# Performance work log

Hardware: AMD Instinct MI355X
Metric: run time of the kernel (lower is better)

Reference implementation:

```python
import jax, jax.numpy as jnp
import numpy as np

NEG_INF = -1e30  # masked_softmax fill (squad util convention)


def setup_inputs() -> dict:
    key = jax.random.key(0)
    ks = jax.random.split(key, 5)
    B, S, H = 4, 2048, 512
    x = jax.random.normal(ks[0], (B, S, H), dtype=jnp.float32)
    mask = jax.random.randint(ks[1], (B, S), 0, 2, dtype=jnp.int32)
    mask = mask.at[:, 0].set(1)  # ensure at least one valid key per row
    W_comb = jax.random.normal(ks[2], (H, 3 * H), dtype=jnp.float32) * (1.0 / np.sqrt(H))
    b_comb = jnp.zeros((3 * H,), dtype=jnp.float32)
    W_out = jax.random.normal(ks[3], (H, H), dtype=jnp.float32) * (1.0 / np.sqrt(H))
    b_out = jnp.zeros((H,), dtype=jnp.float32)
    return {"x": x, "mask": mask, "W_comb": W_comb, "b_comb": b_comb,
            "W_out": W_out, "b_out": b_out}


def reference(x, mask, W_comb, b_comb, W_out, b_out):
    B, S, H = x.shape
    n_head = 8
    d = H // n_head
    scale = d ** 0.5
    qkv = x @ W_comb + b_comb                      # [B,S,3H]
    q, k, v = jnp.split(qkv, 3, axis=-1)
    q = q.reshape(B, S, n_head, d)
    k = k.reshape(B, S, n_head, d)
    v = v.reshape(B, S, n_head, d)
    # [B,h,Sq,Sk] scores; mask applies along the key axis
    scores = jnp.einsum('bqhd,bkhd->bhqk', q / scale, k)
    key_mask = (mask > 0)[:, None, None, :]        # [B,1,1,Sk]
    logits = jnp.where(key_mask, scores, NEG_INF)
    attn = jax.nn.softmax(logits, axis=-1)         # dropout = identity (eval)
    out = jnp.einsum('bhqk,bkhd->bqhd', attn, v).reshape(B, S, H)
    return out @ W_out + b_out
```

## Files before the change

### kernel.cpp

```cpp
#include <hip/hip_runtime.h>
#include <hip/hip_bf16.h>
#include <stdint.h>

typedef unsigned short u16;
typedef unsigned int u32;
typedef __attribute__((ext_vector_type(8))) __bf16 bf16x8;
typedef __attribute__((ext_vector_type(8))) unsigned short us8;
typedef __attribute__((ext_vector_type(4))) unsigned short us4;
typedef __attribute__((ext_vector_type(4))) float f32x4;
typedef __attribute__((ext_vector_type(16))) float f32x16;
typedef __attribute__((ext_vector_type(4))) unsigned int u32x4;
typedef __attribute__((ext_vector_type(2))) unsigned int u32x2;

#define KSCALE_Q 0.18033688011112042f

#define VMCNT(n) asm volatile("s_waitcnt vmcnt(" #n ")" ::: "memory")
#define BARRIER() __builtin_amdgcn_s_barrier()

__device__ inline u16 f2bf(float f) {
  union { __bf16 b; u16 s; } x; x.b = (__bf16)f; return x.s;
}
__device__ inline u32 packbf(float a, float b) {
  return (u32)f2bf(a) | ((u32)f2bf(b) << 16);
}
__device__ inline f32x16 zero16() {
  f32x16 z; for (int i = 0; i < 16; ++i) z[i] = 0.f; return z;
}
__device__ __forceinline__ void gl_lds16(const u16* g, u16* l) {
  __builtin_amdgcn_global_load_lds(
      (const __attribute__((address_space(1))) void*)g,
      (__attribute__((address_space(3))) void*)l, 16, 0, 0);
}
__device__ __forceinline__ void pl32swap(u32& a, u32& b) {
#if __has_builtin(__builtin_amdgcn_permlane32_swap)
  u32x2 r = __builtin_amdgcn_permlane32_swap(a, b, false, false);
  a = r[0]; b = r[1];
#else
  u32 ta = (u32)__shfl_xor((int)a, 32);
  u32 tb = (u32)__shfl_xor((int)b, 32);
  int hi = (threadIdx.x & 63) >> 5;
  u32 na = hi ? tb : a;
  u32 nb = hi ? b : ta;
  a = na; b = nb;
#endif
}

__global__ __launch_bounds__(256) void prep(
    const float* __restrict__ x, const float* __restrict__ Wc,
    const float* __restrict__ Wo, const int* __restrict__ mask,
    u16* __restrict__ xbf, u16* __restrict__ wct, u16* __restrict__ wot,
    int* __restrict__ idx, int* __restrict__ nbv) {
  int r = blockIdx.x, tid = threadIdx.x;
  if (r < 4096) {
    int i = r * 256 + tid;
    float4 v = ((const float4*)x)[i];
    us4 o;
    o[0] = f2bf(v.x); o[1] = f2bf(v.y); o[2] = f2bf(v.z); o[3] = f2bf(v.w);
    ((us4*)xbf)[i] = o;
    return;
  }
  __shared__ float tile[32][33];
  __shared__ int ps[256];
  if (r < 5120) {
    const float* in; u16* outT; int R, C, bi;
    if (r < 4864) { in = Wc; outT = wct; R = 512; C = 1536; bi = r - 4096; }
    else          { in = Wo; outT = wot; R = 512; C = 512;  bi = r - 4864; }
    int nbx = C >> 5;
    int bx = bi % nbx, by = bi / nbx;
    int xq = tid & 31, yq = tid >> 5;
    int c0 = bx * 32, r0 = by * 32;
    for (int j = 0; j < 32; j += 8)
      tile[yq + j][xq] = in[(size_t)(r0 + yq + j) * C + c0 + xq];
    __syncthreads();
    for (int j = 0; j < 32; j += 8)
      outT[(size_t)(c0 + yq + j) * R + r0 + xq] = f2bf(tile[xq][yq + j]);
    return;
  }
  int b = r - 5120;
  const int* mrow = mask + b * 2048;
  int4 a = ((const int4*)mrow)[tid * 2];
  int4 c = ((const int4*)mrow)[tid * 2 + 1];
  int v[8] = {a.x, a.y, a.z, a.w, c.x, c.y, c.z, c.w};
  int cnt = 0;
  for (int i = 0; i < 8; ++i) cnt += (v[i] > 0);
  ps[tid] = cnt;
  __syncthreads();
  for (int off = 1; off < 256; off <<= 1) {
    int xv = ps[tid];
    int yv = (tid >= off) ? ps[tid - off] : 0;
    __syncthreads();
    ps[tid] = xv + yv;
    __syncthreads();
  }
  int total = ps[255];
  int pos = ps[tid] - cnt;
  int* ip = idx + b * 2048;
  for (int i = 0; i < 8; ++i)
    if (v[i] > 0) ip[pos++] = tid * 8 + i;
  for (int i = 0; i < 8; ++i) {
    int j = tid * 8 + i;
    if (j >= total) ip[j] = 0;
  }
  if (tid == 0) nbv[b] = total;
}

__global__ __launch_bounds__(256) void gemm_qkv(
    const u16* __restrict__ A, const u16* __restrict__ Bt,
    const float* __restrict__ bias, u16* __restrict__ Qc,
    u16* __restrict__ Kc, u16* __restrict__ VTc,
    const int* __restrict__ idx, const int* __restrict__ nbv) {
  const int K = 512;
  int bid = blockIdx.x;
  bool isQ = bid < 256;
  int b = 0, m0, n0;
  if (isQ) {
    m0 = (bid >> 2) * 128;
    n0 = (bid & 3) * 128;
  } else {
    int t = bid - 256;
    b = t >> 7;
    int rr_ = t & 127;
    m0 = (rr_ & 15) * 128;
    n0 = (rr_ >> 4) * 128 + 512;
    int npad = (nbv[b] + 127) & ~127;
    if (m0 >= npad) return;
  }
  __shared__ __align__(16) u16 As[2][128 * 64];
  __shared__ __align__(16) u16 Bs[2][128 * 64];
  int tid = threadIdx.x, wave = tid >> 6, lane = tid & 63;
  int quad = lane >> 4, l16 = lane & 15;
  int wm = (wave >> 1) * 64, wn = (wave & 1) * 64;

  int r8 = lane >> 3;
  int cb = (lane & 7) ^ r8;
  const u16* agp[4];
  for (int i = 0; i < 4; ++i) {
    int row = m0 + wave * 32 + i * 8 + r8;
    int grow = isQ ? row : (b * 2048 + idx[b * 2048 + row]);
    agp[i] = A + (size_t)grow * K + cb * 8;
  }
  const u16* bg = Bt + (size_t)(n0 + wave * 32 + r8) * K + cb * 8;
  int lofs = (wave * 32) * 64 + lane * 8;

  f32x4 acc[4][4];
  for (int i = 0; i < 4; ++i)
    for (int j = 0; j < 4; ++j) acc[i][j] = (f32x4){0.f, 0.f, 0.f, 0.f};

  int rx = l16 & 7;

  auto stage = [&](int buf, int kk) {
    u16* al = As[buf] + lofs;
    u16* bl = Bs[buf] + lofs;
#pragma unroll
    for (int i = 0; i < 4; ++i)
      gl_lds16(agp[i] + kk, al + i * 8 * 64);
#pragma unroll
    for (int i = 0; i < 4; ++i)
      gl_lds16(bg + kk + (size_t)(i * 8) * K, bl + i * 8 * 64);
  };

  stage(0, 0);
  for (int t = 0; t < 8; ++t) {
    if (t < 7) { stage((t + 1) & 1, (t + 1) * 64); VMCNT(8); }
    else       { VMCNT(0); }
    BARRIER();
    const u16* Asb = As[t & 1];
    const u16* Bsb = Bs[t & 1];
#pragma unroll
    for (int ks = 0; ks < 2; ++ks) {
      int pos = ((ks * 4 + quad) ^ rx) * 8;
      bf16x8 af[4], bfr[4];
#pragma unroll
      for (int i = 0; i < 4; ++i)
        af[i] = *(const bf16x8*)(Asb + (wm + i * 16 + l16) * 64 + pos);
#pragma unroll
      for (int j = 0; j < 4; ++j)
        bfr[j] = *(const bf16x8*)(Bsb + (wn + j * 16 + l16) * 64 + pos);
#pragma unroll
      for (int i = 0; i < 4; ++i)
#pragma unroll
        for (int j = 0; j < 4; ++j)
          acc[i][j] = __builtin_amdgcn_mfma_f32_16x16x32_bf16(
              af[i], bfr[j], acc[i][j], 0, 0, 0);
    }
    BARRIER();
  }
  for (int j = 0; j < 4; ++j) {
    int col = n0 + wn + j * 16 + l16;
    float bv = bias[col];
    if (isQ) {
      for (int i = 0; i < 4; ++i) {
        int rowb = m0 + wm + i * 16 + quad * 4;
        for (int rr = 0; rr < 4; ++rr)
          Qc[(size_t)(rowb + rr) * 512 + col] =
              f2bf((acc[i][j][rr] + bv) * KSCALE_Q);
      }
    } else if (col < 1024) {
      int ck = col - 512;
      for (int i = 0; i < 4; ++i) {
        int key0 = m0 + wm + i * 16 + quad * 4;
        for (int rr = 0; rr < 4; ++rr)
          Kc[((size_t)b * 2048 + key0 + rr) * 512 + ck] =
              f2bf(acc[i][j][rr] + bv);
      }
    } else {
      int hd = col - 1024;
      int h = hd >> 6, d = hd & 63;
      u16* vrow = VTc + ((size_t)(b * 8 + h) * 64 + d) * 2048;
      for (int i = 0; i < 4; ++i) {
        int key0 = m0 + wm + i * 16 + quad * 4;
        us4 pk;
        for (int rr = 0; rr < 4; ++rr) pk[rr] = f2bf(acc[i][j][rr] + bv);
        *(us4*)(vrow + key0) = pk;
      }
    }
  }
}

__global__ __launch_bounds__(256) void gemm_out(
    const u16* __restrict__ A, const u16* __restrict__ Bt,
    const float* __restrict__ bias, float* __restrict__ Cout) {
  const int K = 512, N = 512;
  int m0 = blockIdx.y * 128, n0 = blockIdx.x * 128;
  __shared__ __align__(16) u16 As[2][128 * 64];
  __shared__ __align__(16) u16 Bs[2][128 * 64];
  int tid = threadIdx.x, wave = tid >> 6, lane = tid & 63;
  int quad = lane >> 4, l16 = lane & 15;
  int wm = (wave >> 1) * 64, wn = (wave & 1) * 64;

  int r8 = lane >> 3;
  int cb = (lane & 7) ^ r8;
  const u16* ag = A + (size_t)(m0 + wave * 32 + r8) * K + cb * 8;
  const u16* bg = Bt + (size_t)(n0 + wave * 32 + r8) * K + cb * 8;
  int lofs = (wave * 32) * 64 + lane * 8;

  f32x4 acc[4][4];
  for (int i = 0; i < 4; ++i)
    for (int j = 0; j < 4; ++j) acc[i][j] = (f32x4){0.f, 0.f, 0.f, 0.f};

  int rx = l16 & 7;

  auto stage = [&](int buf, int kk) {
    u16* al = As[buf] + lofs;
    u16* bl = Bs[buf] + lofs;
#pragma unroll
    for (int i = 0; i < 4; ++i)
      gl_lds16(ag + kk + (size_t)(i * 8) * K, al + i * 8 * 64);
#pragma unroll
    for (int i = 0; i < 4; ++i)
      gl_lds16(bg + kk + (size_t)(i * 8) * K, bl + i * 8 * 64);
  };

  stage(0, 0);
  for (int t = 0; t < 8; ++t) {
    if (t < 7) { stage((t + 1) & 1, (t + 1) * 64); VMCNT(8); }
    else       { VMCNT(0); }
    BARRIER();
    const u16* Asb = As[t & 1];
    const u16* Bsb = Bs[t & 1];
#pragma unroll
    for (int ks = 0; ks < 2; ++ks) {
      int pos = ((ks * 4 + quad) ^ rx) * 8;
      bf16x8 af[4], bfr[4];
#pragma unroll
      for (int i = 0; i < 4; ++i)
        af[i] = *(const bf16x8*)(Asb + (wm + i * 16 + l16) * 64 + pos);
#pragma unroll
      for (int j = 0; j < 4; ++j)
        bfr[j] = *(const bf16x8*)(Bsb + (wn + j * 16 + l16) * 64 + pos);
#pragma unroll
      for (int i = 0; i < 4; ++i)
#pragma unroll
        for (int j = 0; j < 4; ++j)
          acc[i][j] = __builtin_amdgcn_mfma_f32_16x16x32_bf16(
              af[i], bfr[j], acc[i][j], 0, 0, 0);
    }
    BARRIER();
  }
  for (int j = 0; j < 4; ++j) {
    int col = n0 + wn + j * 16 + l16;
    float bv = bias[col];
    for (int i = 0; i < 4; ++i) {
      int rowb = m0 + wm + i * 16 + quad * 4;
      for (int rr = 0; rr < 4; ++rr)
        Cout[(size_t)(rowb + rr) * N + col] = acc[i][j][rr] + bv;
    }
  }
}

__global__ __launch_bounds__(256) void attn_kernel(
    const u16* __restrict__ Qc, const u16* __restrict__ Kc,
    const u16* __restrict__ VTc, const int* __restrict__ nbv,
    u16* __restrict__ aout) {
  int b = blockIdx.z, h = blockIdx.y, q0 = blockIdx.x * 256;
  int bh = b * 8 + h;
  int tid = threadIdx.x, wave = tid >> 6, lane = tid & 63;
  int l5 = lane & 31, hi = lane >> 5;
  int nb = nbv[b];
  int npad = (nb + 127) & ~127;
  int NT = npad >> 7;

  __shared__ __align__(16) u16 Kt[2][128 * 64];
  __shared__ __align__(16) u16 Vt[2][64 * 128];

  bf16x8 qf[2][4];
#pragma unroll
  for (int qg = 0; qg < 2; ++qg) {
    int qrow = b * 2048 + q0 + wave * 64 + qg * 32 + l5;
#pragma unroll
    for (int s = 0; s < 4; ++s)
      qf[qg][s] = *(const bf16x8*)(Qc + (size_t)qrow * 512 + h * 64 + s * 16 +
                                   hi * 8);
  }
  VMCNT(0);

  f32x16 o[2][2];
#pragma unroll
  for (int qg = 0; qg < 2; ++qg)
#pragma unroll
    for (int dc = 0; dc < 2; ++dc) o[qg][dc] = zero16();
  float lsum[2] = {0.f, 0.f};

  int krr = lane >> 3;
  int kcb = (lane & 7) ^ krr;
  const u16* kg = Kc + ((size_t)(b * 2048) + wave * 32 + krr) * 512 + h * 64 +
                  kcb * 8;
  int vrr = lane >> 4;

  auto stageKV = [&](int buf, int kt0) {
    u16* kl = Kt[buf] + (wave * 32) * 64 + lane * 8;
#pragma unroll
    for (int i = 0; i < 4; ++i)
      gl_lds16(kg + (size_t)(kt0 + i * 8) * 512, kl + i * 8 * 64);
    u16* vl = Vt[buf] + (wave * 16) * 128 + lane * 8;
#pragma unroll
    for (int i = 0; i < 4; ++i) {
      int vr = wave * 16 + i * 4 + vrr;
      int vcb = (lane & 15) ^ (vr & 15);
      gl_lds16(VTc + ((size_t)(bh * 64) + vr) * 2048 + kt0 + vcb * 8,
               vl + i * 4 * 128);
    }
  };

  stageKV(0, 0);
  for (int t = 0; t < NT; ++t) {
    if (t + 1 < NT) { stageKV((t + 1) & 1, (t + 1) * 128); VMCNT(8); }
    else            { VMCNT(0); }
    BARRIER();
    const u16* Ktc = Kt[t & 1];
    const u16* Vtc = Vt[t & 1];
    int kt0 = t * 128;
    bool maskT = (kt0 + 128 > nb);

#pragma unroll
    for (int kg4 = 0; kg4 < 4; ++kg4) {
      int krow = kg4 * 32 + l5;
      const u16* kro = Ktc + krow * 64;
      int rx = krow & 7;
      bf16x8 ka[4];
#pragma unroll
      for (int s = 0; s < 4; ++s)
        ka[s] = *(const bf16x8*)(kro + ((s * 2 + hi) ^ rx) * 8);
      f32x16 sa[2];
      sa[0] = zero16(); sa[1] = zero16();
#pragma unroll
      for (int s = 0; s < 4; ++s) {
        sa[0] = __builtin_amdgcn_mfma_f32_32x32x16_bf16(ka[s], qf[0][s],
                                                        sa[0], 0, 0, 0);
        sa[1] = __builtin_amdgcn_mfma_f32_32x32x16_bf16(ka[s], qf[1][s],
                                                        sa[1], 0, 0, 0);
      }
      bf16x8 pb[2][2];
#pragma unroll
      for (int qg = 0; qg < 2; ++qg) {
        if (maskT) {
#pragma unroll
          for (int r = 0; r < 16; ++r) {
            int jg = kt0 + kg4 * 32 + (r & 3) + 8 * (r >> 2) + 4 * hi;
            if (jg >= nb) sa[qg][r] = -1e30f;
          }
        }
        u32 pk[8];
        float ls = 0.f;
#pragma unroll
        for (int j = 0; j < 8; ++j) {
          float e0 = __builtin_amdgcn_exp2f(sa[qg][2 * j]);
          float e1 = __builtin_amdgcn_exp2f(sa[qg][2 * j + 1]);
          ls += e0 + e1;
          pk[j] = packbf(e0, e1);
        }
        lsum[qg] += ls;
#pragma unroll
        for (int t2 = 0; t2 < 2; ++t2) {
          u32 a0 = pk[t2 * 4 + 0], a2 = pk[t2 * 4 + 2];
          u32 a1 = pk[t2 * 4 + 1], a3 = pk[t2 * 4 + 3];
          pl32swap(a0, a2);
          pl32swap(a1, a3);
          u32x4 qv; qv[0] = a0; qv[1] = a1; qv[2] = a2; qv[3] = a3;
          pb[qg][t2] = __builtin_bit_cast(bf16x8, qv);
        }
      }
#pragma unroll
      for (int t2 = 0; t2 < 2; ++t2) {
        int cblk = kg4 * 4 + t2 * 2 + hi;
#pragma unroll
        for (int dc = 0; dc < 2; ++dc) {
          int vrow = dc * 32 + l5;
          bf16x8 va = *(const bf16x8*)(Vtc + vrow * 128 +
                                       ((cblk ^ (vrow & 15)) * 8));
          o[0][dc] = __builtin_amdgcn_mfma_f32_32x32x16_bf16(
              va, pb[0][t2], o[0][dc], 0, 0, 0);
          o[1][dc] = __builtin_amdgcn_mfma_f32_32x32x16_bf16(
              va, pb[1][t2], o[1][dc], 0, 0, 0);
        }
      }
    }
    BARRIER();
  }

#pragma unroll
  for (int qg = 0; qg < 2; ++qg) {
    float lt = lsum[qg];
    lt += __shfl_xor(lt, 32);
    float inv = 1.f / lt;
    int qrow = b * 2048 + q0 + wave * 64 + qg * 32 + l5;
#pragma unroll
    for (int dc = 0; dc < 2; ++dc)
#pragma unroll
      for (int mI = 0; mI < 4; ++mI) {
        us4 pk;
        for (int r = 0; r < 4; ++r) pk[r] = f2bf(o[qg][dc][mI * 4 + r] * inv);
        *(us4*)(aout + (size_t)qrow * 512 + h * 64 + dc * 32 + mI * 8 +
                hi * 4) = pk;
      }
  }
}

extern "C" void kernel_launch(void* const* d_in, const int* in_sizes, int n_in,
                              void* d_out, int out_size, void* d_ws,
                              size_t ws_size, hipStream_t stream) {
  const float* x = (const float*)d_in[0];
  const int* mask = (const int*)d_in[1];
  const float* Wc = (const float*)d_in[2];
  const float* bc = (const float*)d_in[3];
  const float* Wo = (const float*)d_in[4];
  const float* bo = (const float*)d_in[5];
  float* out = (float*)d_out;

  char* ws = (char*)d_ws;
  u16* xbf = (u16*)(ws);
  u16* wct = (u16*)(ws + 8388608);
  u16* wot = (u16*)(ws + 9961472);
  u16* Qc  = (u16*)(ws + 10485760);
  u16* Kc  = (u16*)(ws + 18874368);
  u16* vtc = (u16*)(ws + 27262976);
  int* idx = (int*)(ws + 35651584);
  int* nbv = (int*)(ws + 35684352);
  u16* aout = xbf;

  prep<<<5124, 256, 0, stream>>>(x, Wc, Wo, mask, xbf, wct, wot, idx, nbv);
  gemm_qkv<<<768, 256, 0, stream>>>(xbf, wct, bc, Qc, Kc, vtc, idx, nbv);
  attn_kernel<<<dim3(8, 8, 4), 256, 0, stream>>>(Qc, Kc, vtc, nbv, aout);
  gemm_out<<<dim3(4, 64), 256, 0, stream>>>(aout, wot, bo, out);
}
```

Measured before the change: 152.4 us.

## Split attention key range across two wave groups with LDS reduction

Doubles the attention block to 512 threads. The two groups of four waves each process half of the key tiles for the same 256 queries, with separate double-buffered K/V tiles in shared memory. Partial outputs and row sums from the second group are then reduced through shared memory before normalisation and the store. This targets low occupancy: only 256 blocks of 4 waves were available on a large GPU. The cost is doubled LDS per block, an extra reduction pass, and barriers that are now shared across both groups.

```diff
diff --git a/kernel.cpp b/kernel.cpp
--- a/kernel.cpp
+++ b/kernel.cpp
@@ -288,25 +288,29 @@
   }
 }
 
-__global__ __launch_bounds__(256) void attn_kernel(
+__global__ __launch_bounds__(512, 2) void attn_kernel(
     const u16* __restrict__ Qc, const u16* __restrict__ Kc,
     const u16* __restrict__ VTc, const int* __restrict__ nbv,
     u16* __restrict__ aout) {
   int b = blockIdx.z, h = blockIdx.y, q0 = blockIdx.x * 256;
   int bh = b * 8 + h;
   int tid = threadIdx.x, wave = tid >> 6, lane = tid & 63;
+  int g = wave >> 2, sw = wave & 3;
   int l5 = lane & 31, hi = lane >> 5;
   int nb = nbv[b];
   int npad = (nb + 127) & ~127;
   int NT = npad >> 7;
-
-  __shared__ __align__(16) u16 Kt[2][128 * 64];
-  __shared__ __align__(16) u16 Vt[2][64 * 128];
+  int NT0 = (NT + 1) >> 1;
+  int NTg = g ? (NT - NT0) : NT0;
+  int tb = g ? NT0 : 0;
+
+  __shared__ __align__(16) u16 Kt[2][2][128 * 64];
+  __shared__ __align__(16) u16 Vt[2][2][64 * 128];
 
   bf16x8 qf[2][4];
 #pragma unroll
   for (int qg = 0; qg < 2; ++qg) {
-    int qrow = b * 2048 + q0 + wave * 64 + qg * 32 + l5;
+    int qrow = b * 2048 + q0 + sw * 64 + qg * 32 + l5;
 #pragma unroll
     for (int s = 0; s < 4; ++s)
       qf[qg][s] = *(const bf16x8*)(Qc + (size_t)qrow * 512 + h * 64 + s * 16 +
@@ -323,116 +327,154 @@
 
   int krr = lane >> 3;
   int kcb = (lane & 7) ^ krr;
-  const u16* kg = Kc + ((size_t)(b * 2048) + wave * 32 + krr) * 512 + h * 64 +
+  const u16* kg = Kc + ((size_t)(b * 2048) + sw * 32 + krr) * 512 + h * 64 +
                   kcb * 8;
   int vrr = lane >> 4;
 
   auto stageKV = [&](int buf, int kt0) {
-    u16* kl = Kt[buf] + (wave * 32) * 64 + lane * 8;
+    u16* kl = Kt[g][buf] + (sw * 32) * 64 + lane * 8;
 #pragma unroll
     for (int i = 0; i < 4; ++i)
       gl_lds16(kg + (size_t)(kt0 + i * 8) * 512, kl + i * 8 * 64);
-    u16* vl = Vt[buf] + (wave * 16) * 128 + lane * 8;
+    u16* vl = Vt[g][buf] + (sw * 16) * 128 + lane * 8;
 #pragma unroll
     for (int i = 0; i < 4; ++i) {
-      int vr = wave * 16 + i * 4 + vrr;
+      int vr = sw * 16 + i * 4 + vrr;
       int vcb = (lane & 15) ^ (vr & 15);
       gl_lds16(VTc + ((size_t)(bh * 64) + vr) * 2048 + kt0 + vcb * 8,
                vl + i * 4 * 128);
     }
   };
 
-  stageKV(0, 0);
-  for (int t = 0; t < NT; ++t) {
-    if (t + 1 < NT) { stageKV((t + 1) & 1, (t + 1) * 128); VMCNT(8); }
-    else            { VMCNT(0); }
+  if (NTg > 0) stageKV(0, tb * 128);
+  for (int t = 0; t < NT0; ++t) {
+    if (t + 1 < NTg)  { stageKV((t + 1) & 1, (tb + t + 1) * 128); VMCNT(8); }
+    else if (t < NTg) { VMCNT(0); }
     BARRIER();
-    const u16* Ktc = Kt[t & 1];
-    const u16* Vtc = Vt[t & 1];
-    int kt0 = t * 128;
-    bool maskT = (kt0 + 128 > nb);
-
-#pragma unroll
-    for (int kg4 = 0; kg4 < 4; ++kg4) {
-      int krow = kg4 * 32 + l5;
-      const u16* kro = Ktc + krow * 64;
-      int rx = krow & 7;
-      bf16x8 ka[4];
-#pragma unroll
-      for (int s = 0; s < 4; ++s)
-        ka[s] = *(const bf16x8*)(kro + ((s * 2 + hi) ^ rx) * 8);
-      f32x16 sa[2];
-      sa[0] = zero16(); sa[1] = zero16();
-#pragma unroll
-      for (int s = 0; s < 4; ++s) {
-        sa[0] = __builtin_amdgcn_mfma_f32_32x32x16_bf16(ka[s], qf[0][s],
-                                                        sa[0], 0, 0, 0);
-        sa[1] = __builtin_amdgcn_mfma_f32_32x32x16_bf16(ka[s], qf[1][s],
-                                                        sa[1], 0, 0, 0);
-      }
-      bf16x8 pb[2][2];
-#pragma unroll
-      for (int qg = 0; qg < 2; ++qg) {
-        if (maskT) {
-#pragma unroll
-          for (int r = 0; r < 16; ++r) {
-            int jg = kt0 + kg4 * 32 + (r & 3) + 8 * (r >> 2) + 4 * hi;
-            if (jg >= nb) sa[qg][r] = -1e30f;
+    if (t < NTg) {
+      const u16* Ktc = Kt[g][t & 1];
+      const u16* Vtc = Vt[g][t & 1];
+      int kt0 = (tb + t) * 128;
+      bool maskT = (kt0 + 128 > nb);
+
+#pragma unroll
+      for (int kg4 = 0; kg4 < 4; ++kg4) {
+        int krow = kg4 * 32 + l5;
+        const u16* kro = Ktc + krow * 64;
+        int rx = krow & 7;
+        bf16x8 ka[4];
+#pragma unroll
+        for (int s = 0; s < 4; ++s)
+          ka[s] = *(const bf16x8*)(kro + ((s * 2 + hi) ^ rx) * 8);
+        f32x16 sa[2];
+        sa[0] = zero16(); sa[1] = zero16();
+#pragma unroll
+        for (int s = 0; s < 4; ++s) {
+          sa[0] = __builtin_amdgcn_mfma_f32_32x32x16_bf16(ka[s], qf[0][s],
+                                                          sa[0], 0, 0, 0);
+          sa[1] = __builtin_amdgcn_mfma_f32_32x32x16_bf16(ka[s], qf[1][s],
+                                                          sa[1], 0, 0, 0);
+        }
+        bf16x8 pb[2][2];
+#pragma unroll
+        for (int qg = 0; qg < 2; ++qg) {
+          if (maskT) {
+#pragma unroll
+            for (int r = 0; r < 16; ++r) {
+              int jg = kt0 + kg4 * 32 + (r & 3) + 8 * (r >> 2) + 4 * hi;
+              if (jg >= nb) sa[qg][r] = -1e30f;
+            }
+          }
+          u32 pk[8];
+          float ls = 0.f;
+#pragma unroll
+          for (int j = 0; j < 8; ++j) {
+            float e0 = __builtin_amdgcn_exp2f(sa[qg][2 * j]);
+            float e1 = __builtin_amdgcn_exp2f(sa[qg][2 * j + 1]);
+            ls += e0 + e1;
+            pk[j] = packbf(e0, e1);
+          }
+          lsum[qg] += ls;
+#pragma unroll
+          for (int t2 = 0; t2 < 2; ++t2) {
+            u32 a0 = pk[t2 * 4 + 0], a2 = pk[t2 * 4 + 2];
+            u32 a1 = pk[t2 * 4 + 1], a3 = pk[t2 * 4 + 3];
+            pl32swap(a0, a2);
+            pl32swap(a1, a3);
+            u32x4 qv; qv[0] = a0; qv[1] = a1; qv[2] = a2; qv[3] = a3;
+            pb[qg][t2] = __builtin_bit_cast(bf16x8, qv);
           }
         }
-        u32 pk[8];
-        float ls = 0.f;
-#pragma unroll
-        for (int j = 0; j < 8; ++j) {
-          float e0 = __builtin_amdgcn_exp2f(sa[qg][2 * j]);
-          float e1 = __builtin_amdgcn_exp2f(sa[qg][2 * j + 1]);
-          ls += e0 + e1;
-          pk[j] = packbf(e0, e1);
-        }
-        lsum[qg] += ls;
 #pragma unroll
         for (int t2 = 0; t2 < 2; ++t2) {
-          u32 a0 = pk[t2 * 4 + 0], a2 = pk[t2 * 4 + 2];
-          u32 a1 = pk[t2 * 4 + 1], a3 = pk[t2 * 4 + 3];
-          pl32swap(a0, a2);
-          pl32swap(a1, a3);
-          u32x4 qv; qv[0] = a0; qv[1] = a1; qv[2] = a2; qv[3] = a3;
-          pb[qg][t2] = __builtin_bit_cast(bf16x8, qv);
+          int cblk = kg4 * 4 + t2 * 2 + hi;
+#pragma unroll
+          for (int dc = 0; dc < 2; ++dc) {
+            int vrow = dc * 32 + l5;
+            bf16x8 va = *(const bf16x8*)(Vtc + vrow * 128 +
+                                         ((cblk ^ (vrow & 15)) * 8));
+            o[0][dc] = __builtin_amdgcn_mfma_f32_32x32x16_bf16(
+                va, pb[0][t2], o[0][dc], 0, 0, 0);
+            o[1][dc] = __builtin_amdgcn_mfma_f32_32x32x16_bf16(
+                va, pb[1][t2], o[1][dc], 0, 0, 0);
+          }
         }
       }
-#pragma unroll
-      for (int t2 = 0; t2 < 2; ++t2) {
-        int cblk = kg4 * 4 + t2 * 2 + hi;
-#pragma unroll
-        for (int dc = 0; dc < 2; ++dc) {
-          int vrow = dc * 32 + l5;
-          bf16x8 va = *(const bf16x8*)(Vtc + vrow * 128 +
-                                       ((cblk ^ (vrow & 15)) * 8));
-          o[0][dc] = __builtin_amdgcn_mfma_f32_32x32x16_bf16(
-              va, pb[0][t2], o[0][dc], 0, 0, 0);
-          o[1][dc] = __builtin_amdgcn_mfma_f32_32x32x16_bf16(
-              va, pb[1][t2], o[1][dc], 0, 0, 0);
+    }
+    BARRIER();
+  }
+
+  float* xch = (float*)(&Kt[0][0][0]);
+  float* xls = (float*)(&Vt[0][0][0]);
+  if (g == 1) {
+    float* dst = xch + sw * 4096 + lane * 4;
+#pragma unroll
+    for (int qg = 0; qg < 2; ++qg)
+#pragma unroll
+      for (int dc = 0; dc < 2; ++dc)
+#pragma unroll
+        for (int r4 = 0; r4 < 4; ++r4) {
+          int c = qg * 8 + dc * 4 + r4;
+          f32x4 v;
+          for (int r = 0; r < 4; ++r) v[r] = o[qg][dc][r4 * 4 + r];
+          *(f32x4*)(dst + c * 256) = v;
         }
-      }
-    }
-    BARRIER();
-  }
-
-#pragma unroll
-  for (int qg = 0; qg < 2; ++qg) {
-    float lt = lsum[qg];
-    lt += __shfl_xor(lt, 32);
-    float inv = 1.f / lt;
-    int qrow = b * 2048 + q0 + wave * 64 + qg * 32 + l5;
-#pragma unroll
-    for (int dc = 0; dc < 2; ++dc)
-#pragma unroll
-      for (int mI = 0; mI < 4; ++mI) {
-        us4 pk;
-        for (int r = 0; r < 4; ++r) pk[r] = f2bf(o[qg][dc][mI * 4 + r] * inv);
-        *(us4*)(aout + (size_t)qrow * 512 + h * 64 + dc * 32 + mI * 8 +
-                hi * 4) = pk;
-      }
+    xls[sw * 128 + lane * 2 + 0] = lsum[0];
+    xls[sw * 128 + lane * 2 + 1] = lsum[1];
+  }
+  __syncthreads();
+  if (g == 0) {
+    const float* src = xch + sw * 4096 + lane * 4;
+#pragma unroll
+    for (int qg = 0; qg < 2; ++qg)
+#pragma unroll
+      for (int dc = 0; dc < 2; ++dc)
+#pragma unroll
+        for (int r4 = 0; r4 < 4; ++r4) {
+          int c = qg * 8 + dc * 4 + r4;
+          f32x4 v = *(const f32x4*)(src + c * 256);
+          for (int r = 0; r < 4; ++r) o[qg][dc][r4 * 4 + r] += v[r];
+        }
+    lsum[0] += xls[sw * 128 + lane * 2 + 0];
+    lsum[1] += xls[sw * 128 + lane * 2 + 1];
+
+#pragma unroll
+    for (int qg = 0; qg < 2; ++qg) {
+      float lt = lsum[qg];
+      lt += __shfl_xor(lt, 32);
+      float inv = 1.f / lt;
+      int qrow = b * 2048 + q0 + sw * 64 + qg * 32 + l5;
+#pragma unroll
+      for (int dc = 0; dc < 2; ++dc)
+#pragma unroll
+        for (int mI = 0; mI < 4; ++mI) {
+          us4 pk;
+          for (int r = 0; r < 4; ++r)
+            pk[r] = f2bf(o[qg][dc][mI * 4 + r] * inv);
+          *(us4*)(aout + (size_t)qrow * 512 + h * 64 + dc * 32 + mI * 8 +
+                  hi * 4) = pk;
+        }
+    }
   }
 }
 
@@ -460,6 +502,6 @@
 
   prep<<<5124, 256, 0, stream>>>(x, Wc, Wo, mask, xbf, wct, wot, idx, nbv);
   gemm_qkv<<<768, 256, 0, stream>>>(xbf, wct, bc, Qc, Kc, vtc, idx, nbv);
-  attn_kernel<<<dim3(8, 8, 4), 256, 0, stream>>>(Qc, Kc, vtc, nbv, aout);
+  attn_kernel<<<dim3(8, 8, 4), 512, 0, stream>>>(Qc, Kc, vtc, nbv, aout);
   gemm_out<<<dim3(4, 64), 256, 0, stream>>>(aout, wot, bo, out);
 }
```

New measurement: 159.8 us. +4.9%, slower.

## Halve attention query tile, double grid, add XCD-aware block remap

Applied to the files above, without the earlier changes.

The attention kernel now gives each block 128 queries (32 per wave) instead of 256, which doubles the grid from 256 to 512 blocks. The grid is flattened and remapped so blocks of the same batch and head land on the same XCD, aiming for better L2 reuse of K/V. The inner loop is restructured to process two 32-key chunks per step against one query group, and launch_bounds asks for 2 blocks per CU. Each K/V tile is now loaded by twice as many blocks, which raises global and LDS traffic per query in exchange for better CU occupancy and load balance on the 256-CU device.

```diff
diff --git a/kernel.cpp b/kernel.cpp
--- a/kernel.cpp
+++ b/kernel.cpp
@@ -288,11 +288,15 @@
   }
 }
 
-__global__ __launch_bounds__(256) void attn_kernel(
+__global__ __launch_bounds__(256, 2) void attn_kernel(
     const u16* __restrict__ Qc, const u16* __restrict__ Kc,
     const u16* __restrict__ VTc, const int* __restrict__ nbv,
     u16* __restrict__ aout) {
-  int b = blockIdx.z, h = blockIdx.y, q0 = blockIdx.x * 256;
+  int flat = blockIdx.x;
+  int xcd = flat & 7, ii = flat >> 3;
+  int p = ((ii >> 4) << 3) | xcd;
+  int c = ii & 15;
+  int b = p >> 3, h = p & 7, q0 = c * 128;
   int bh = b * 8 + h;
   int tid = threadIdx.x, wave = tid >> 6, lane = tid & 63;
   int l5 = lane & 31, hi = lane >> 5;
@@ -303,23 +307,17 @@
   __shared__ __align__(16) u16 Kt[2][128 * 64];
   __shared__ __align__(16) u16 Vt[2][64 * 128];
 
-  bf16x8 qf[2][4];
-#pragma unroll
-  for (int qg = 0; qg < 2; ++qg) {
-    int qrow = b * 2048 + q0 + wave * 64 + qg * 32 + l5;
-#pragma unroll
-    for (int s = 0; s < 4; ++s)
-      qf[qg][s] = *(const bf16x8*)(Qc + (size_t)qrow * 512 + h * 64 + s * 16 +
-                                   hi * 8);
-  }
+  bf16x8 qf[4];
+  int qrow = b * 2048 + q0 + wave * 32 + l5;
+#pragma unroll
+  for (int s = 0; s < 4; ++s)
+    qf[s] = *(const bf16x8*)(Qc + (size_t)qrow * 512 + h * 64 + s * 16 +
+                             hi * 8);
   VMCNT(0);
 
-  f32x16 o[2][2];
-#pragma unroll
-  for (int qg = 0; qg < 2; ++qg)
-#pragma unroll
-    for (int dc = 0; dc < 2; ++dc) o[qg][dc] = zero16();
-  float lsum[2] = {0.f, 0.f};
+  f32x16 o[2];
+  o[0] = zero16(); o[1] = zero16();
+  float lsum = 0.f;
 
   int krr = lane >> 3;
   int kcb = (lane & 7) ^ krr;
@@ -342,6 +340,7 @@
     }
   };
 
+  int rx = l5 & 7;
   stageKV(0, 0);
   for (int t = 0; t < NT; ++t) {
     if (t + 1 < NT) { stageKV((t + 1) & 1, (t + 1) * 128); VMCNT(8); }
@@ -353,43 +352,45 @@
     bool maskT = (kt0 + 128 > nb);
 
 #pragma unroll
-    for (int kg4 = 0; kg4 < 4; ++kg4) {
-      int krow = kg4 * 32 + l5;
-      const u16* kro = Ktc + krow * 64;
-      int rx = krow & 7;
-      bf16x8 ka[4];
-#pragma unroll
-      for (int s = 0; s < 4; ++s)
-        ka[s] = *(const bf16x8*)(kro + ((s * 2 + hi) ^ rx) * 8);
+    for (int kp = 0; kp < 2; ++kp) {
+      bf16x8 ka[2][4];
+#pragma unroll
+      for (int cc = 0; cc < 2; ++cc) {
+        const u16* kro = Ktc + ((kp * 2 + cc) * 32 + l5) * 64;
+#pragma unroll
+        for (int s = 0; s < 4; ++s)
+          ka[cc][s] = *(const bf16x8*)(kro + ((s * 2 + hi) ^ rx) * 8);
+      }
       f32x16 sa[2];
       sa[0] = zero16(); sa[1] = zero16();
 #pragma unroll
       for (int s = 0; s < 4; ++s) {
-        sa[0] = __builtin_amdgcn_mfma_f32_32x32x16_bf16(ka[s], qf[0][s],
+        sa[0] = __builtin_amdgcn_mfma_f32_32x32x16_bf16(ka[0][s], qf[s],
                                                         sa[0], 0, 0, 0);
-        sa[1] = __builtin_amdgcn_mfma_f32_32x32x16_bf16(ka[s], qf[1][s],
+        sa[1] = __builtin_amdgcn_mfma_f32_32x32x16_bf16(ka[1][s], qf[s],
                                                         sa[1], 0, 0, 0);
       }
       bf16x8 pb[2][2];
 #pragma unroll
-      for (int qg = 0; qg < 2; ++qg) {
+      for (int cc = 0; cc < 2; ++cc) {
+        int kg4 = kp * 2 + cc;
         if (maskT) {
 #pragma unroll
           for (int r = 0; r < 16; ++r) {
             int jg = kt0 + kg4 * 32 + (r & 3) + 8 * (r >> 2) + 4 * hi;
-            if (jg >= nb) sa[qg][r] = -1e30f;
+            if (jg >= nb) sa[cc][r] = -1e30f;
           }
         }
         u32 pk[8];
         float ls = 0.f;
 #pragma unroll
         for (int j = 0; j < 8; ++j) {
-          float e0 = __builtin_amdgcn_exp2f(sa[qg][2 * j]);
-          float e1 = __builtin_amdgcn_exp2f(sa[qg][2 * j + 1]);
+          float e0 = __builtin_amdgcn_exp2f(sa[cc][2 * j]);
+          float e1 = __builtin_amdgcn_exp2f(sa[cc][2 * j + 1]);
           ls += e0 + e1;
           pk[j] = packbf(e0, e1);
         }
-        lsum[qg] += ls;
+        lsum += ls;
 #pragma unroll
         for (int t2 = 0; t2 < 2; ++t2) {
           u32 a0 = pk[t2 * 4 + 0], a2 = pk[t2 * 4 + 2];
@@ -397,43 +398,41 @@
           pl32swap(a0, a2);
           pl32swap(a1, a3);
           u32x4 qv; qv[0] = a0; qv[1] = a1; qv[2] = a2; qv[3] = a3;
-          pb[qg][t2] = __builtin_bit_cast(bf16x8, qv);
+          pb[cc][t2] = __builtin_bit_cast(bf16x8, qv);
         }
       }
 #pragma unroll
-      for (int t2 = 0; t2 < 2; ++t2) {
-        int cblk = kg4 * 4 + t2 * 2 + hi;
-#pragma unroll
-        for (int dc = 0; dc < 2; ++dc) {
-          int vrow = dc * 32 + l5;
-          bf16x8 va = *(const bf16x8*)(Vtc + vrow * 128 +
-                                       ((cblk ^ (vrow & 15)) * 8));
-          o[0][dc] = __builtin_amdgcn_mfma_f32_32x32x16_bf16(
-              va, pb[0][t2], o[0][dc], 0, 0, 0);
-          o[1][dc] = __builtin_amdgcn_mfma_f32_32x32x16_bf16(
-              va, pb[1][t2], o[1][dc], 0, 0, 0);
+      for (int cc = 0; cc < 2; ++cc) {
+        int kg4 = kp * 2 + cc;
+#pragma unroll
+        for (int t2 = 0; t2 < 2; ++t2) {
+          int cblk = kg4 * 4 + t2 * 2 + hi;
+#pragma unroll
+          for (int dc = 0; dc < 2; ++dc) {
+            int vrow = dc * 32 + l5;
+            bf16x8 va = *(const bf16x8*)(Vtc + vrow * 128 +
+                                         ((cblk ^ (vrow & 15)) * 8));
+            o[dc] = __builtin_amdgcn_mfma_f32_32x32x16_bf16(
+                va, pb[cc][t2], o[dc], 0, 0, 0);
+          }
         }
       }
     }
     BARRIER();
   }
 
-#pragma unroll
-  for (int qg = 0; qg < 2; ++qg) {
-    float lt = lsum[qg];
-    lt += __shfl_xor(lt, 32);
-    float inv = 1.f / lt;
-    int qrow = b * 2048 + q0 + wave * 64 + qg * 32 + l5;
-#pragma unroll
-    for (int dc = 0; dc < 2; ++dc)
-#pragma unroll
-      for (int mI = 0; mI < 4; ++mI) {
-        us4 pk;
-        for (int r = 0; r < 4; ++r) pk[r] = f2bf(o[qg][dc][mI * 4 + r] * inv);
-        *(us4*)(aout + (size_t)qrow * 512 + h * 64 + dc * 32 + mI * 8 +
-                hi * 4) = pk;
-      }
-  }
+  float lt = lsum;
+  lt += __shfl_xor(lt, 32);
+  float inv = 1.f / lt;
+#pragma unroll
+  for (int dc = 0; dc < 2; ++dc)
+#pragma unroll
+    for (int mI = 0; mI < 4; ++mI) {
+      us4 pk;
+      for (int r = 0; r < 4; ++r) pk[r] = f2bf(o[dc][mI * 4 + r] * inv);
+      *(us4*)(aout + (size_t)qrow * 512 + h * 64 + dc * 32 + mI * 8 +
+              hi * 4) = pk;
+    }
 }
 
 extern "C" void kernel_launch(void* const* d_in, const int* in_sizes, int n_in,
@@ -460,6 +459,6 @@
 
   prep<<<5124, 256, 0, stream>>>(x, Wc, Wo, mask, xbf, wct, wot, idx, nbv);
   gemm_qkv<<<768, 256, 0, stream>>>(xbf, wct, bc, Qc, Kc, vtc, idx, nbv);
-  attn_kernel<<<dim3(8, 8, 4), 256, 0, stream>>>(Qc, Kc, vtc, nbv, aout);
+  attn_kernel<<<512, 256, 0, stream>>>(Qc, Kc, vtc, nbv, aout);
   gemm_out<<<dim3(4, 64), 256, 0, stream>>>(aout, wot, bo, out);
 }
```

Result: faster. 144.2 us (-5.4%).
